# Performance work log

Hardware: AMD Instinct MI355X
Metric: run time of the kernel (lower is better)

The kernel has to match this reference:

```python
import jax, jax.numpy as jnp
import numpy as np

B, L, D = 2, 2048, 2048
H, HKV, HD = 32, 8, 64
EPS = 1e-5
THETA = 1000000.0


def rms_norm(x, w):
    # normalize over last dim (head_dim)
    return x * jax.lax.rsqrt(jnp.mean(x * x, axis=-1, keepdims=True) + EPS) * w


def apply_rope(t):
    # t: (B, heads, L, HD); non-traditional (half-split) RoPE, offset=0
    half = HD // 2
    inv_freq = THETA ** (-jnp.arange(0, HD, 2, dtype=jnp.float32) / HD)  # (half,)
    ang = jnp.arange(L, dtype=jnp.float32)[:, None] * inv_freq           # (L, half)
    cos, sin = jnp.cos(ang), jnp.sin(ang)
    x1, x2 = t[..., :half], t[..., half:]
    return jnp.concatenate([x1 * cos - x2 * sin, x2 * cos + x1 * sin], axis=-1)


def setup_inputs() -> dict:
    key = jax.random.key(0)
    ks = jax.random.split(key, 5)
    s = 0.02
    return {
        "x": jax.random.normal(ks[0], (B, L, D), dtype=jnp.float32),
        "Wq": jax.random.normal(ks[1], (D, H * HD), dtype=jnp.float32) * s,
        "Wk": jax.random.normal(ks[2], (D, HKV * HD), dtype=jnp.float32) * s,
        "Wv": jax.random.normal(ks[3], (D, HKV * HD), dtype=jnp.float32) * s,
        "Wo": jax.random.normal(ks[4], (H * HD, D), dtype=jnp.float32) * s,
        "q_norm_w": jnp.ones((HD,), dtype=jnp.float32),
        "k_norm_w": jnp.ones((HD,), dtype=jnp.float32),
    }


def reference(x, Wq, Wk, Wv, Wo, q_norm_w, k_norm_w):
    scale = HD ** -0.5
    g = H // HKV  # GQA group size
    # projections
    q = (x @ Wq).reshape(B, L, H, HD)
    k = (x @ Wk).reshape(B, L, HKV, HD)
    v = (x @ Wv).reshape(B, L, HKV, HD)
    # per-head RMSNorm, then to (B, heads, L, HD)
    q = jnp.transpose(rms_norm(q, q_norm_w), (0, 2, 1, 3))
    k = jnp.transpose(rms_norm(k, k_norm_w), (0, 2, 1, 3))
    v = jnp.transpose(v, (0, 2, 1, 3))
    # RoPE
    q = apply_rope(q)
    k = apply_rope(k)
    # grouped-query attention with causal mask
    qg = q.reshape(B, HKV, g, L, HD)
    scores = jnp.einsum('bhgqd,bhkd->bhgqk', qg, k) * scale  # (B,HKV,g,L,L)
    causal = jnp.tril(jnp.ones((L, L), dtype=bool))
    scores = jnp.where(causal, scores, jnp.finfo(scores.dtype).min)
    probs = jax.nn.softmax(scores, axis=-1)
    out = jnp.einsum('bhgqk,bhkd->bhgqd', probs, v)           # (B,HKV,g,L,HD)
    out = jnp.transpose(out.reshape(B, H, L, HD), (0, 2, 1, 3)).reshape(B, L, H * HD)
    return out @ Wo
```

## Files before the change

### kernel.cpp

```cpp
#include <hip/hip_runtime.h>
#include <math.h>
#include <stdint.h>

#define B_ 2
#define L_ 2048
#define D_ 2048
#define H_ 32
#define HKV_ 8
#define HD_ 64
#define EPS_ 1e-5f

typedef _Float16 half_t;
typedef __attribute__((ext_vector_type(8))) _Float16 half8_t;
typedef __attribute__((ext_vector_type(4))) _Float16 half4_t;
typedef __attribute__((ext_vector_type(4))) float float4_t;

typedef const __attribute__((address_space(1))) uint32_t glb_u32;
typedef __attribute__((address_space(3))) uint32_t lds_u32;
#define GLOAD_LDS16(gp, lp) \
  __builtin_amdgcn_global_load_lds((glb_u32*)(gp), (lds_u32*)(lp), 16, 0, 0)

__device__ __forceinline__ float4_t fmax4(float4_t a, float4_t b) {
  float4_t r;
  r[0] = fmaxf(a[0], b[0]); r[1] = fmaxf(a[1], b[1]);
  r[2] = fmaxf(a[2], b[2]); r[3] = fmaxf(a[3], b[3]);
  return r;
}

__device__ __forceinline__ uint32_t pk_f16(float a, float b) {
  auto p = __builtin_amdgcn_cvt_pkrtz(a, b);
  return __builtin_bit_cast(uint32_t, p);
}

__global__ __launch_bounds__(256) void prep_all(
    const float* __restrict__ x,
    const float* __restrict__ Wq, const float* __restrict__ Wk,
    const float* __restrict__ Wv, const float* __restrict__ Wo,
    half_t* __restrict__ xh,
    half_t* __restrict__ Wqt, half_t* __restrict__ Wkt,
    half_t* __restrict__ Wvt, half_t* __restrict__ Wot)
{
  __shared__ float tile[64][65];
  const int t = threadIdx.x;
  int id = blockIdx.x;

  if (id < 4096) {
    size_t i = ((size_t)id * 256 + t) * 8;
    float4 v0 = *(const float4*)&x[i];
    float4 v1 = *(const float4*)&x[i + 4];
    half8_t h;
    h[0] = (half_t)v0.x; h[1] = (half_t)v0.y; h[2] = (half_t)v0.z; h[3] = (half_t)v0.w;
    h[4] = (half_t)v1.x; h[5] = (half_t)v1.y; h[6] = (half_t)v1.z; h[7] = (half_t)v1.w;
    *(half8_t*)&xh[i] = h;
    return;
  }
  id -= 4096;
  const float* W; half_t* Wt; int N;
  if (id < 1024)      { W = Wq; Wt = Wqt; N = 2048; }
  else if (id < 1280) { id -= 1024; W = Wk; Wt = Wkt; N = 512; }
  else if (id < 1536) { id -= 1280; W = Wv; Wt = Wvt; N = 512; }
  else                { id -= 1536; W = Wo; Wt = Wot; N = 2048; }
  const int K = 2048;
  int tk = id & 31, tn = id >> 5;
  int k0 = tk * 64, n0 = tn * 64;

  int rr = t >> 6, cc = t & 63;
#pragma unroll
  for (int i = 0; i < 16; i++)
    tile[rr + i * 4][cc] = W[(size_t)(k0 + rr + i * 4) * N + n0 + cc];
  __syncthreads();

  int rn = t >> 2, q4 = (t & 3) * 16;
  half8_t h0, h1;
#pragma unroll
  for (int u = 0; u < 8; u++) h0[u] = (half_t)tile[q4 + u][rn];
#pragma unroll
  for (int u = 0; u < 8; u++) h1[u] = (half_t)tile[q4 + 8 + u][rn];
  *(half8_t*)&Wt[(size_t)(n0 + rn) * K + k0 + q4]     = h0;
  *(half8_t*)&Wt[(size_t)(n0 + rn) * K + k0 + q4 + 8] = h1;
}

__global__ __launch_bounds__(256) void build_trig(
    float* __restrict__ ct, float* __restrict__ st)
{
  int e = blockIdx.x * 256 + threadIdx.x;
  int l = e >> 5, fi = e & 31;
  float inv_freq = exp2f((float)fi * -0.622862853f);
  float ang = (float)l * inv_freq;
  ct[e] = cosf(ang);
  st[e] = sinf(ang);
}

template <typename CT>
__device__ __forceinline__ void gemm_tile_f16(
    const half_t* __restrict__ A, const half_t* __restrict__ Bt,
    CT* __restrict__ C, int K, int ldc, int row0, int col0)
{
  __shared__ __align__(16) half_t As[128 * 32];
  __shared__ __align__(16) half_t Bs[128 * 32];
  const int t    = threadIdx.x;
  const int lane = t & 63;
  const int w    = t >> 6;
  const int quad = lane >> 4, c = lane & 15;
  const int wm = (w >> 1) * 64, wn = (w & 1) * 64;

  float4_t acc[4][4];
#pragma unroll
  for (int i = 0; i < 4; i++)
#pragma unroll
    for (int j = 0; j < 4; j++) acc[i][j] = (float4_t){0.f, 0.f, 0.f, 0.f};

  const int srow = w * 32 + (lane >> 2);
  const int scol = (lane & 3) * 8;
  const half_t* Ag0 = A  + (size_t)(row0 + srow) * K + scol;
  const half_t* Ag1 = Ag0 + (size_t)16 * K;
  const half_t* Bg0 = Bt + (size_t)(col0 + srow) * K + scol;
  const half_t* Bg1 = Bg0 + (size_t)16 * K;
  half_t* As_w0 = &As[(w * 32) * 32];
  half_t* As_w1 = &As[(w * 32 + 16) * 32];
  half_t* Bs_w0 = &Bs[(w * 32) * 32];
  half_t* Bs_w1 = &Bs[(w * 32 + 16) * 32];

  for (int k0 = 0; k0 < K; k0 += 32) {
    __syncthreads();
    GLOAD_LDS16(Ag0 + k0, As_w0);
    GLOAD_LDS16(Ag1 + k0, As_w1);
    GLOAD_LDS16(Bg0 + k0, Bs_w0);
    GLOAD_LDS16(Bg1 + k0, Bs_w1);
    __syncthreads();

    half8_t af[4], bf[4];
#pragma unroll
    for (int i = 0; i < 4; i++)
      af[i] = *(const half8_t*)&As[(wm + i * 16 + c) * 32 + quad * 8];
#pragma unroll
    for (int j = 0; j < 4; j++)
      bf[j] = *(const half8_t*)&Bs[(wn + j * 16 + c) * 32 + quad * 8];
#pragma unroll
    for (int i = 0; i < 4; i++)
#pragma unroll
      for (int j = 0; j < 4; j++)
        acc[i][j] = __builtin_amdgcn_mfma_f32_16x16x32_f16(af[i], bf[j], acc[i][j], 0, 0, 0);
  }

#pragma unroll
  for (int i = 0; i < 4; i++)
#pragma unroll
    for (int r = 0; r < 4; r++) {
      CT* Cp = C + (size_t)(row0 + wm + i * 16 + quad * 4 + r) * ldc + col0 + wn + c;
#pragma unroll
      for (int j = 0; j < 4; j++)
        Cp[j * 16] = (CT)acc[i][j][r];
    }
}

__global__ __launch_bounds__(256) void qkv_gemm_h(
    const half_t* __restrict__ xh,
    const half_t* __restrict__ Wqt, const half_t* __restrict__ Wkt,
    const half_t* __restrict__ Wvt,
    half_t* __restrict__ qh, half_t* __restrict__ kh, half_t* __restrict__ vh)
{
  int lin = (int)blockIdx.y * 24 + (int)blockIdx.x;
  int xcd = lin & 7, idx = lin >> 3;
  int cy = xcd >> 2, cx = xcd & 3;
  int by = cy * 16 + idx / 6;
  int bx = cx * 6 + idx % 6;

  const half_t* Bt; half_t* C; int ldc, col0;
  if (bx < 16)      { Bt = Wqt; C = qh; ldc = H_ * HD_;   col0 = bx * 128; }
  else if (bx < 20) { Bt = Wkt; C = kh; ldc = HKV_ * HD_; col0 = (bx - 16) * 128; }
  else              { Bt = Wvt; C = vh; ldc = HKV_ * HD_; col0 = (bx - 20) * 128; }
  gemm_tile_f16<half_t>(xh, Bt, C, D_, ldc, by * 128, col0);
}

__global__ __launch_bounds__(256) void out_gemm_h(
    const half_t* __restrict__ attn, const half_t* __restrict__ Wot,
    float* __restrict__ out)
{
  int lin = (int)blockIdx.y * 16 + (int)blockIdx.x;
  int xcd = lin & 7, idx = lin >> 3;
  int cy = xcd >> 1, cx = xcd & 1;
  int by = cy * 8 + idx / 8;
  int bx = cx * 8 + idx % 8;
  gemm_tile_f16<float>(attn, Wot, out, H_ * HD_, D_, by * 128, bx * 128);
}

__device__ __forceinline__ void norm_rope_row(
    half_t* __restrict__ buf, float wv, int row, int nheads, int lognh,
    int lane, float oscale, float cv, float sv)
{
  int head  = row & (nheads - 1);
  int token = row >> lognh;

  size_t idx = (size_t)token * (nheads * HD_) + head * HD_ + lane;
  float x = (float)buf[idx];

  float ss = x * x;
#pragma unroll
  for (int off = 32; off; off >>= 1) ss += __shfl_xor(ss, off);
  float xn = x * rsqrtf(ss * (1.0f / HD_) + EPS_) * wv;

  float partner = __shfl_xor(xn, 32);
  float res = (lane < 32) ? (xn * cv - partner * sv) : (xn * cv + partner * sv);
  buf[idx] = (half_t)(res * oscale);
}

__global__ __launch_bounds__(256) void postproc(
    half_t* __restrict__ qh, half_t* __restrict__ kh,
    const half_t* __restrict__ vh, half_t* __restrict__ vt,
    const float* __restrict__ qw, const float* __restrict__ kw,
    const float* __restrict__ ct, const float* __restrict__ st)
{
  const int t    = threadIdx.x;
  const int lane = t & 63;
  const int wv   = t >> 6;
  int id = blockIdx.x;

  if (id < 8192) {
    int row0  = (id * 4 + wv) * 4;
    int token = row0 >> 5;
    int l     = token & (L_ - 1);
    float cvv = ct[l * 32 + (lane & 31)];
    float svv = st[l * 32 + (lane & 31)];
    float wq  = qw[lane];
#pragma unroll
    for (int u = 0; u < 4; u++)
      norm_rope_row(qh, wq, row0 + u, H_, 5, lane, 0.180336880f, cvv, svv);
    return;
  }
  id -= 8192;
  if (id < 2048) {
    int row0  = (id * 4 + wv) * 4;
    int token = row0 >> 3;
    int l     = token & (L_ - 1);
    float cvv = ct[l * 32 + (lane & 31)];
    float svv = st[l * 32 + (lane & 31)];
    float wk  = kw[lane];
#pragma unroll
    for (int u = 0; u < 4; u++)
      norm_rope_row(kh, wk, row0 + u, HKV_, 3, lane, 1.0f, cvv, svv);
    return;
  }
  id -= 2048;
  int kk0 = (id & 31) * 64, kvh = (id >> 5) & 7, b = id >> 8;
  int d = t >> 2, uu = t & 3;
  const half_t* src = vh + (size_t)(b * L_) * (HKV_ * HD_) + kvh * HD_ + d;
  half_t* dst = vt + ((size_t)((b * HKV_ + kvh) * HD_ + d)) * L_ + kk0 + uu * 16;
  half_t vals[16];
#pragma unroll
  for (int u = 0; u < 16; u++)
    vals[u] = src[(size_t)(kk0 + uu * 16 + u) * (HKV_ * HD_)];
#pragma unroll
  for (int u = 0; u < 16; u += 4)
    *(half4_t*)&dst[u] = *(half4_t*)&vals[u];
}

__global__ __launch_bounds__(512) void flash_mfma2(
    const half_t* __restrict__ Qh, const half_t* __restrict__ Kh,
    const half_t* __restrict__ Vt, half_t* __restrict__ Oa)
{
  __shared__ __align__(16) half_t Ks[64][72];
  __shared__ __align__(16) half_t Vs[64][72];
  __shared__ __align__(16) half_t Ps[128][72];
  __shared__ __align__(16) float  Ab[128];

  const int t    = threadIdx.x;
  const int w    = t >> 6;
  const int lane = t & 63;
  const int quad = lane >> 4;
  const int c    = lane & 15;
  const int h = blockIdx.y, b = blockIdx.z;
  const int kvh = h >> 2;

  const half_t* kbase = Kh + (size_t)(b * L_) * (HKV_ * HD_) + kvh * HD_;
  const half_t* vbase = Vt + (size_t)((b * HKV_ + kvh) * HD_) * L_;
  const int sr = t >> 3;
  const int su = (t & 7) * 8;

  half8_t ones;
#pragma unroll
  for (int u = 0; u < 8; u++) ones[u] = (half_t)1.0f;

  for (int pass = 0; pass < 2; pass++) {
    const int qb  = pass ? (15 - (int)blockIdx.x) : (int)blockIdx.x;
    const int q0  = qb * 128;
    const int wq0 = q0 + w * 16;

    half8_t qf0, qf1;
    {
      const half_t* qp = Qh + ((size_t)(b * L_ + wq0 + c)) * (H_ * HD_) + h * HD_;
      qf0 = *(const half8_t*)&qp[quad * 8];
      qf1 = *(const half8_t*)&qp[32 + quad * 8];
    }

    float4_t o[5];
#pragma unroll
    for (int dt = 0; dt < 5; dt++) o[dt] = (float4_t){0.f, 0.f, 0.f, 0.f};
    float mm = -__builtin_inff();

    half8_t kr, vr;
    kr = *(const half8_t*)(kbase + (size_t)sr * (HKV_ * HD_) + su);
    vr = *(const half8_t*)(vbase + (size_t)sr * L_ + su);

    const int last = (q0 + 127) >> 6;
    for (int kt = 0; kt <= last; kt++) {
      const int kk0 = kt * 64;
      __syncthreads();
      *(half8_t*)&Ks[sr][su] = kr;
      *(half8_t*)&Vs[sr][su] = vr;
      __syncthreads();
      if (kt < last) {
        kr = *(const half8_t*)(kbase + (size_t)(kk0 + 64 + sr) * (HKV_ * HD_) + su);
        vr = *(const half8_t*)(vbase + (size_t)sr * L_ + kk0 + 64 + su);
      }
      if (kk0 > wq0 + 15) continue;

      float4_t S[4];
      __builtin_amdgcn_s_setprio(1);
#pragma unroll
      for (int tt = 0; tt < 4; tt++) {
        half8_t kf0 = *(const half8_t*)&Ks[tt * 16 + c][quad * 8];
        half8_t kf1 = *(const half8_t*)&Ks[tt * 16 + c][32 + quad * 8];
        float4_t s = (float4_t){0.f, 0.f, 0.f, 0.f};
        s = __builtin_amdgcn_mfma_f32_16x16x32_f16(kf0, qf0, s, 0, 0, 0);
        s = __builtin_amdgcn_mfma_f32_16x16x32_f16(kf1, qf1, s, 0, 0, 0);
        S[tt] = s;
      }
      __builtin_amdgcn_s_setprio(0);

      if (kk0 + 63 > wq0) {
#pragma unroll
        for (int tt = 0; tt < 4; tt++) {
          int base = kk0 + tt * 16 + quad * 4 - (wq0 + c);
#pragma unroll
          for (int r = 0; r < 4; r++)
            if (base + r > 0) S[tt][r] = -__builtin_inff();
        }
      }

      {
        float4_t m4 = fmax4(fmax4(S[0], S[1]), fmax4(S[2], S[3]));
        float mloc = fmaxf(fmaxf(m4[0], m4[1]), fmaxf(m4[2], m4[3]));
        mloc = fmaxf(mloc, __shfl_xor(mloc, 16));
        mloc = fmaxf(mloc, __shfl_xor(mloc, 32));
        if (__any(mloc > mm + 8.0f)) {
          float mnew = fmaxf(mm, mloc);
          float al = exp2f(mm - mnew);
          mm = mnew;
          if (quad == 0) Ab[w * 16 + c] = al;
          float4_t av = *(const float4_t*)&Ab[w * 16 + quad * 4];
#pragma unroll
          for (int dt = 0; dt < 5; dt++)
#pragma unroll
            for (int r = 0; r < 4; r++) o[dt][r] *= av[r];
        }
#pragma unroll
        for (int tt = 0; tt < 4; tt++) {
#pragma unroll
          for (int r = 0; r < 4; r++) S[tt][r] = exp2f(S[tt][r] - mm);
          uint2 pw;
          pw.x = pk_f16(S[tt][0], S[tt][1]);
          pw.y = pk_f16(S[tt][2], S[tt][3]);
          *(uint2*)&Ps[w * 16 + c][tt * 16 + quad * 4] = pw;
        }
      }

      half8_t pf0 = *(const half8_t*)&Ps[w * 16 + c][quad * 8];
      half8_t pf1 = *(const half8_t*)&Ps[w * 16 + c][32 + quad * 8];
      __builtin_amdgcn_s_setprio(1);
      o[4] = __builtin_amdgcn_mfma_f32_16x16x32_f16(pf0, ones, o[4], 0, 0, 0);
      o[4] = __builtin_amdgcn_mfma_f32_16x16x32_f16(pf1, ones, o[4], 0, 0, 0);
#pragma unroll
      for (int dt = 0; dt < 4; dt++) {
        half8_t vf0 = *(const half8_t*)&Vs[dt * 16 + c][quad * 8];
        half8_t vf1 = *(const half8_t*)&Vs[dt * 16 + c][32 + quad * 8];
        o[dt] = __builtin_amdgcn_mfma_f32_16x16x32_f16(pf0, vf0, o[dt], 0, 0, 0);
        o[dt] = __builtin_amdgcn_mfma_f32_16x16x32_f16(pf1, vf1, o[dt], 0, 0, 0);
      }
      __builtin_amdgcn_s_setprio(0);
    }

#pragma unroll
    for (int r = 0; r < 4; r++) {
      float inv = 1.0f / o[4][r];
      half_t* op = Oa + ((size_t)(b * L_ + wq0 + quad * 4 + r)) * (H_ * HD_)
                 + h * HD_ + c;
#pragma unroll
      for (int dt = 0; dt < 4; dt++)
        op[dt * 16] = (half_t)(o[dt][r] * inv);
    }
  }
}

extern "C" void kernel_launch(void* const* d_in, const int* in_sizes, int n_in,
                              void* d_out, int out_size, void* d_ws, size_t ws_size,
                              hipStream_t stream)
{
  const float* x  = (const float*)d_in[0];
  const float* Wq = (const float*)d_in[1];
  const float* Wk = (const float*)d_in[2];
  const float* Wv = (const float*)d_in[3];
  const float* Wo = (const float*)d_in[4];
  const float* qw = (const float*)d_in[5];
  const float* kw = (const float*)d_in[6];
  float* out = (float*)d_out;

  const size_t XN = (size_t)B_ * L_ * D_;
  const size_t QN = (size_t)B_ * L_ * H_ * HD_;
  const size_t KN = (size_t)B_ * L_ * HKV_ * HD_;
  const size_t WQ = (size_t)D_ * H_ * HD_;
  const size_t WK = (size_t)D_ * HKV_ * HD_;

  half_t* p   = (half_t*)d_ws;
  half_t* xh  = p;  p += XN;
  half_t* Wqt = p;  p += WQ;
  half_t* Wkt = p;  p += WK;
  half_t* Wvt = p;  p += WK;
  half_t* Wot = p;  p += WQ;
  half_t* qh  = p;  p += QN;
  half_t* kh  = p;  p += KN;
  half_t* vh  = p;  p += KN;
  half_t* vt  = p;  p += KN;
  half_t* attn = xh;

  float* ct = (float*)Wqt;
  float* st = ct + 65536;

  prep_all<<<6656, 256, 0, stream>>>(x, Wq, Wk, Wv, Wo, xh, Wqt, Wkt, Wvt, Wot);

  qkv_gemm_h<<<dim3(24, 32), 256, 0, stream>>>(xh, Wqt, Wkt, Wvt, qh, kh, vh);

  build_trig<<<256, 256, 0, stream>>>(ct, st);

  postproc<<<8192 + 2048 + 512, 256, 0, stream>>>(qh, kh, vh, vt, qw, kw, ct, st);

  flash_mfma2<<<dim3(8, H_, B_), 512, 0, stream>>>(qh, kh, vt, attn);

  out_gemm_h<<<dim3(16, 32), 256, 0, stream>>>(attn, Wot, out);
}
```

Measured before the change: 317.0 us.

## Fuse V transpose into QKV GEMM epilogue and compute RoPE trig inline

The V projection tiles of the QKV GEMM now write their outputs directly in transposed (head, dim, token) layout, which removes the separate V transpose pass inside postproc and the intermediate vh buffer. The build_trig kernel is also dropped, and cos/sin are computed inline in postproc instead of being loaded from a table. Together these remove one launch, one pass over V, and the trig table traffic. In exchange, the GEMM epilogue does strided half4 stores for V, and postproc spends extra ALU on sin/cos.

```diff
diff --git a/kernel.cpp b/kernel.cpp
--- a/kernel.cpp
+++ b/kernel.cpp
@@ -80,21 +80,11 @@
   *(half8_t*)&Wt[(size_t)(n0 + rn) * K + k0 + q4 + 8] = h1;
 }
 
-__global__ __launch_bounds__(256) void build_trig(
-    float* __restrict__ ct, float* __restrict__ st)
-{
-  int e = blockIdx.x * 256 + threadIdx.x;
-  int l = e >> 5, fi = e & 31;
-  float inv_freq = exp2f((float)fi * -0.622862853f);
-  float ang = (float)l * inv_freq;
-  ct[e] = cosf(ang);
-  st[e] = sinf(ang);
-}
-
 template <typename CT>
 __device__ __forceinline__ void gemm_tile_f16(
     const half_t* __restrict__ A, const half_t* __restrict__ Bt,
-    CT* __restrict__ C, int K, int ldc, int row0, int col0)
+    CT* __restrict__ C, int K, int ldc, int row0, int col0,
+    bool tv, half_t* __restrict__ vtp)
 {
   __shared__ __align__(16) half_t As[128 * 32];
   __shared__ __align__(16) half_t Bs[128 * 32];
@@ -143,22 +133,40 @@
         acc[i][j] = __builtin_amdgcn_mfma_f32_16x16x32_f16(af[i], bf[j], acc[i][j], 0, 0, 0);
   }
 
-#pragma unroll
-  for (int i = 0; i < 4; i++)
-#pragma unroll
-    for (int r = 0; r < 4; r++) {
-      CT* Cp = C + (size_t)(row0 + wm + i * 16 + quad * 4 + r) * ldc + col0 + wn + c;
-#pragma unroll
-      for (int j = 0; j < 4; j++)
-        Cp[j * 16] = (CT)acc[i][j][r];
+  if (tv) {
+    const int kvq = (col0 + wn) >> 6;
+#pragma unroll
+    for (int i = 0; i < 4; i++) {
+      int row = row0 + wm + i * 16 + quad * 4;
+      int bb  = row >> 11;
+      int tok = row & (L_ - 1);
+      half_t* vbase = vtp + (((size_t)bb * HKV_ + kvq) * HD_ + c) * L_ + tok;
+#pragma unroll
+      for (int j = 0; j < 4; j++) {
+        half4_t h4;
+#pragma unroll
+        for (int r = 0; r < 4; r++) h4[r] = (half_t)acc[i][j][r];
+        *(half4_t*)(vbase + (size_t)(j * 16) * L_) = h4;
+      }
     }
+  } else {
+#pragma unroll
+    for (int i = 0; i < 4; i++)
+#pragma unroll
+      for (int r = 0; r < 4; r++) {
+        CT* Cp = C + (size_t)(row0 + wm + i * 16 + quad * 4 + r) * ldc + col0 + wn + c;
+#pragma unroll
+        for (int j = 0; j < 4; j++)
+          Cp[j * 16] = (CT)acc[i][j][r];
+      }
+  }
 }
 
 __global__ __launch_bounds__(256) void qkv_gemm_h(
     const half_t* __restrict__ xh,
     const half_t* __restrict__ Wqt, const half_t* __restrict__ Wkt,
     const half_t* __restrict__ Wvt,
-    half_t* __restrict__ qh, half_t* __restrict__ kh, half_t* __restrict__ vh)
+    half_t* __restrict__ qh, half_t* __restrict__ kh, half_t* __restrict__ vt)
 {
   int lin = (int)blockIdx.y * 24 + (int)blockIdx.x;
   int xcd = lin & 7, idx = lin >> 3;
@@ -166,11 +174,12 @@
   int by = cy * 16 + idx / 6;
   int bx = cx * 6 + idx % 6;
 
-  const half_t* Bt; half_t* C; int ldc, col0;
+  const half_t* Bt; half_t* C; int ldc, col0; bool tv = false;
   if (bx < 16)      { Bt = Wqt; C = qh; ldc = H_ * HD_;   col0 = bx * 128; }
   else if (bx < 20) { Bt = Wkt; C = kh; ldc = HKV_ * HD_; col0 = (bx - 16) * 128; }
-  else              { Bt = Wvt; C = vh; ldc = HKV_ * HD_; col0 = (bx - 20) * 128; }
-  gemm_tile_f16<half_t>(xh, Bt, C, D_, ldc, by * 128, col0);
+  else              { Bt = Wvt; C = vt; ldc = HKV_ * HD_; col0 = (bx - 20) * 128;
+                      tv = true; }
+  gemm_tile_f16<half_t>(xh, Bt, C, D_, ldc, by * 128, col0, tv, vt);
 }
 
 __global__ __launch_bounds__(256) void out_gemm_h(
@@ -182,7 +191,8 @@
   int cy = xcd >> 1, cx = xcd & 1;
   int by = cy * 8 + idx / 8;
   int bx = cx * 8 + idx % 8;
-  gemm_tile_f16<float>(attn, Wot, out, H_ * HD_, D_, by * 128, bx * 128);
+  gemm_tile_f16<float>(attn, Wot, out, H_ * HD_, D_, by * 128, bx * 128,
+                       false, nullptr);
 }
 
 __device__ __forceinline__ void norm_rope_row(
@@ -207,21 +217,22 @@
 
 __global__ __launch_bounds__(256) void postproc(
     half_t* __restrict__ qh, half_t* __restrict__ kh,
-    const half_t* __restrict__ vh, half_t* __restrict__ vt,
-    const float* __restrict__ qw, const float* __restrict__ kw,
-    const float* __restrict__ ct, const float* __restrict__ st)
+    const float* __restrict__ qw, const float* __restrict__ kw)
 {
   const int t    = threadIdx.x;
   const int lane = t & 63;
   const int wv   = t >> 6;
   int id = blockIdx.x;
 
+  int fi = lane & 31;
+  float inv_freq = exp2f((float)fi * -0.622862853f);
+
   if (id < 8192) {
     int row0  = (id * 4 + wv) * 4;
     int token = row0 >> 5;
     int l     = token & (L_ - 1);
-    float cvv = ct[l * 32 + (lane & 31)];
-    float svv = st[l * 32 + (lane & 31)];
+    float ang = (float)l * inv_freq;
+    float cvv = cosf(ang), svv = sinf(ang);
     float wq  = qw[lane];
 #pragma unroll
     for (int u = 0; u < 4; u++)
@@ -229,30 +240,17 @@
     return;
   }
   id -= 8192;
-  if (id < 2048) {
+  {
     int row0  = (id * 4 + wv) * 4;
     int token = row0 >> 3;
     int l     = token & (L_ - 1);
-    float cvv = ct[l * 32 + (lane & 31)];
-    float svv = st[l * 32 + (lane & 31)];
+    float ang = (float)l * inv_freq;
+    float cvv = cosf(ang), svv = sinf(ang);
     float wk  = kw[lane];
 #pragma unroll
     for (int u = 0; u < 4; u++)
       norm_rope_row(kh, wk, row0 + u, HKV_, 3, lane, 1.0f, cvv, svv);
-    return;
-  }
-  id -= 2048;
-  int kk0 = (id & 31) * 64, kvh = (id >> 5) & 7, b = id >> 8;
-  int d = t >> 2, uu = t & 3;
-  const half_t* src = vh + (size_t)(b * L_) * (HKV_ * HD_) + kvh * HD_ + d;
-  half_t* dst = vt + ((size_t)((b * HKV_ + kvh) * HD_ + d)) * L_ + kk0 + uu * 16;
-  half_t vals[16];
-#pragma unroll
-  for (int u = 0; u < 16; u++)
-    vals[u] = src[(size_t)(kk0 + uu * 16 + u) * (HKV_ * HD_)];
-#pragma unroll
-  for (int u = 0; u < 16; u += 4)
-    *(half4_t*)&dst[u] = *(half4_t*)&vals[u];
+  }
 }
 
 __global__ __launch_bounds__(512) void flash_mfma2(
@@ -419,20 +417,14 @@
   half_t* Wot = p;  p += WQ;
   half_t* qh  = p;  p += QN;
   half_t* kh  = p;  p += KN;
-  half_t* vh  = p;  p += KN;
   half_t* vt  = p;  p += KN;
   half_t* attn = xh;
 
-  float* ct = (float*)Wqt;
-  float* st = ct + 65536;
-
   prep_all<<<6656, 256, 0, stream>>>(x, Wq, Wk, Wv, Wo, xh, Wqt, Wkt, Wvt, Wot);
 
-  qkv_gemm_h<<<dim3(24, 32), 256, 0, stream>>>(xh, Wqt, Wkt, Wvt, qh, kh, vh);
-
-  build_trig<<<256, 256, 0, stream>>>(ct, st);
-
-  postproc<<<8192 + 2048 + 512, 256, 0, stream>>>(qh, kh, vh, vt, qw, kw, ct, st);
+  qkv_gemm_h<<<dim3(24, 32), 256, 0, stream>>>(xh, Wqt, Wkt, Wvt, qh, kh, vt);
+
+  postproc<<<8192 + 2048, 256, 0, stream>>>(qh, kh, qw, kw);
 
   flash_mfma2<<<dim3(8, H_, B_), 512, 0, stream>>>(qh, kh, vt, attn);
 
```

Measured after the change: 315.8 us. No clear change (-0.4%).
